# Performance work log

Measured on AMD Instinct MI355X. Metric: run time of the kernel, lower is better.

Reference implementation:

```python
import jax, jax.numpy as jnp
import numpy as np

B, S, D = 64, 4096, 256
LN_EPS = 1e-3  # Keras LayerNormalization default epsilon


def setup_inputs() -> dict:
    key = jax.random.key(0)
    k1, k2, k3 = jax.random.split(key, 3)
    x = jax.random.normal(k1, (B, S, D), dtype=jnp.float32)
    mask = jnp.ones((B, S), dtype=jnp.float32)
    gamma = jnp.ones((D,), dtype=jnp.float32)       # LayerNorm scale
    beta = jnp.zeros((D,), dtype=jnp.float32)       # LayerNorm offset
    w = jax.random.normal(k2, (D,), dtype=jnp.float32) * (1.0 / np.sqrt(D))  # Dense(1) kernel
    b = jnp.zeros((), dtype=jnp.float32)            # Dense(1) bias
    return {"x": x, "mask": mask, "gamma": gamma, "beta": beta, "w": w, "b": b}


def reference(x, mask, gamma, beta, w, b):
    # LayerNorm over feature dim
    mu = jnp.mean(x, axis=-1, keepdims=True)
    var = jnp.mean(jnp.square(x - mu), axis=-1, keepdims=True)
    xn = (x - mu) * jax.lax.rsqrt(var + LN_EPS) * gamma + beta  # [B,S,D]
    # Dense(1) score projection
    score = jnp.einsum('bsd,d->bs', xn, w) + b                  # [B,S]
    # Mask out padded positions, softmax over sequence axis
    score = score + (1.0 - mask) * -1e9
    weights = jax.nn.softmax(score, axis=1)                     # [B,S]
    # Weighted sum over sequence
    return jnp.einsum('bsd,bs->bd', x, weights)                 # [B,D]
```

## Files before the change

kernel.cpp:

```cpp
#include <hip/hip_runtime.h>
#include <math.h>

#define B_   64
#define S_   4096
#define D_   256
#define CH   32
#define ROWS_PER_CHUNK (S_ / CH)
#define NWAVE 4
#define ROWS_PER_BLOCK_ITER (NWAVE * 4)
#define NITER (ROWS_PER_CHUNK / ROWS_PER_BLOCK_ITER)
#define LN_EPS 1e-3f

__global__ __launch_bounds__(256) void pool_pass1(
    const float* __restrict__ x, const float* __restrict__ mask,
    const float* __restrict__ gamma, const float* __restrict__ w,
    float* __restrict__ ws_acc, float* __restrict__ ws_m, float* __restrict__ ws_l)
{
    const int blk   = blockIdx.x;
    const int b     = blk / CH;
    const int chunk = blk % CH;
    const int tid   = threadIdx.x;
    const int lane  = tid & 63;
    const int wave  = tid >> 6;
    const int q     = lane >> 4;
    const int t     = lane & 15;

    float4 gw[4];
    float sgw = 0.0f;
    #pragma unroll
    for (int k = 0; k < 4; ++k) {
        const int d = t * 4 + 64 * k;
        const float4 g4 = *(const float4*)(gamma + d);
        const float4 w4 = *(const float4*)(w + d);
        gw[k].x = g4.x * w4.x; gw[k].y = g4.y * w4.y;
        gw[k].z = g4.z * w4.z; gw[k].w = g4.w * w4.w;
        sgw += gw[k].x + gw[k].y + gw[k].z + gw[k].w;
    }
    #pragma unroll
    for (int off = 8; off > 0; off >>= 1) sgw += __shfl_xor(sgw, off, 64);

    const int row0 = chunk * ROWS_PER_CHUNK + wave * 4 + q;
    const float* xbase = x + ((size_t)b * S_ + row0) * D_ + t * 4;
    const float* mbase = mask + (size_t)b * S_ + row0;

    float  m = -3.0e38f;
    float  l = 0.0f;
    float4 acc[4];
    #pragma unroll
    for (int k = 0; k < 4; ++k) acc[k] = make_float4(0.f, 0.f, 0.f, 0.f);

    float4 v[4];
    #pragma unroll
    for (int k = 0; k < 4; ++k) v[k] = *(const float4*)(xbase + 64 * k);
    float msk = mbase[0];

    for (int i = 0; i < NITER; ++i) {
        const int inx = (i + 1 < NITER) ? i + 1 : i;
        float4 vn[4];
        #pragma unroll
        for (int k = 0; k < 4; ++k)
            vn[k] = *(const float4*)(xbase + (size_t)inx * ROWS_PER_BLOCK_ITER * D_ + 64 * k);
        const float mskn = mbase[inx * ROWS_PER_BLOCK_ITER];

        float s1 = 0.f, s2 = 0.f, s3 = 0.f;
        #pragma unroll
        for (int k = 0; k < 4; ++k) {
            s1 += v[k].x + v[k].y + v[k].z + v[k].w;
            s2 += v[k].x*v[k].x + v[k].y*v[k].y + v[k].z*v[k].z + v[k].w*v[k].w;
            s3 += v[k].x*gw[k].x + v[k].y*gw[k].y + v[k].z*gw[k].z + v[k].w*gw[k].w;
        }
        #pragma unroll
        for (int off = 8; off > 0; off >>= 1) {
            s1 += __shfl_xor(s1, off, 64);
            s2 += __shfl_xor(s2, off, 64);
            s3 += __shfl_xor(s3, off, 64);
        }
        const float mu    = s1 * (1.0f / D_);
        const float var   = s2 * (1.0f / D_) - mu * mu;
        const float rstd  = rsqrtf(var + LN_EPS);
        const float score = rstd * (s3 - mu * sgw) + (1.0f - msk) * -1e9f;

        const float mnew  = fmaxf(m, score);
        const float scale = __expf(m - mnew);
        const float p     = __expf(score - mnew);
        m = mnew;
        l = l * scale + p;
        #pragma unroll
        for (int k = 0; k < 4; ++k) {
            acc[k].x = acc[k].x * scale + p * v[k].x;
            acc[k].y = acc[k].y * scale + p * v[k].y;
            acc[k].z = acc[k].z * scale + p * v[k].z;
            acc[k].w = acc[k].w * scale + p * v[k].w;
        }

        #pragma unroll
        for (int k = 0; k < 4; ++k) v[k] = vn[k];
        msk = mskn;
    }

    __shared__ float s_acc[NWAVE * 4][D_];
    __shared__ float s_m[NWAVE * 4];
    __shared__ float s_l[NWAVE * 4];
    const int g = wave * 4 + q;
    #pragma unroll
    for (int k = 0; k < 4; ++k) *(float4*)&s_acc[g][t * 4 + 64 * k] = acc[k];
    if (t == 0) { s_m[g] = m; s_l[g] = l; }
    __syncthreads();

    float M = -3.0e38f;
    #pragma unroll
    for (int gg = 0; gg < 16; ++gg) M = fmaxf(M, s_m[gg]);
    float L = 0.f, a = 0.f;
    #pragma unroll
    for (int gg = 0; gg < 16; ++gg) {
        const float e = __expf(s_m[gg] - M);
        L += e * s_l[gg];
        a += e * s_acc[gg][tid];
    }
    ws_acc[(size_t)blk * D_ + tid] = a;
    if (tid == 0) { ws_m[blk] = M; ws_l[blk] = L; }
}

__global__ __launch_bounds__(256) void pool_pass2(
    const float* __restrict__ ws_acc, const float* __restrict__ ws_m,
    const float* __restrict__ ws_l, float* __restrict__ out)
{
    const int b = blockIdx.x;
    const int d = threadIdx.x;

    float M = -3.0e38f;
    #pragma unroll
    for (int c = 0; c < CH; ++c) M = fmaxf(M, ws_m[b * CH + c]);

    float L = 0.0f, a = 0.0f;
    #pragma unroll
    for (int c = 0; c < CH; ++c) {
        const float e = __expf(ws_m[b * CH + c] - M);
        L += e * ws_l[b * CH + c];
        a += e * ws_acc[((size_t)(b * CH + c)) * D_ + d];
    }
    out[(size_t)b * D_ + d] = a / L;
}

extern "C" void kernel_launch(void* const* d_in, const int* in_sizes, int n_in,
                              void* d_out, int out_size, void* d_ws, size_t ws_size,
                              hipStream_t stream) {
    const float* x     = (const float*)d_in[0];
    const float* mask  = (const float*)d_in[1];
    const float* gamma = (const float*)d_in[2];
    const float* w     = (const float*)d_in[4];
    float* out = (float*)d_out;

    float* ws_acc = (float*)d_ws;
    float* ws_m   = ws_acc + (size_t)B_ * CH * D_;
    float* ws_l   = ws_m + B_ * CH;

    pool_pass1<<<B_ * CH, 256, 0, stream>>>(x, mask, gamma, w, ws_acc, ws_m, ws_l);
    pool_pass2<<<B_, 256, 0, stream>>>(ws_acc, ws_m, ws_l, out);
}
```

Before: 363.0 us.

## Fuse split-softmax combine into pass1 via last-block atomic counter

Merges the two-kernel split reduction into one kernel. Each block bumps a per-batch atomic counter after writing its partial result, and the last block to finish for that batch does the final cross-chunk combine, which removes the second kernel launch. It also switches the x loads to nontemporal loads and uses ext_vector_type math. A memset of the counters is added on the stream each call, plus threadfence overhead.

```diff
diff --git a/kernel.cpp b/kernel.cpp
--- a/kernel.cpp
+++ b/kernel.cpp
@@ -11,10 +11,13 @@
 #define NITER (ROWS_PER_CHUNK / ROWS_PER_BLOCK_ITER)
 #define LN_EPS 1e-3f
 
-__global__ __launch_bounds__(256) void pool_pass1(
+typedef float f4 __attribute__((ext_vector_type(4)));
+
+__global__ __launch_bounds__(256) void pool_fused(
     const float* __restrict__ x, const float* __restrict__ mask,
     const float* __restrict__ gamma, const float* __restrict__ w,
-    float* __restrict__ ws_acc, float* __restrict__ ws_m, float* __restrict__ ws_l)
+    float* __restrict__ ws_acc, float* __restrict__ ws_m, float* __restrict__ ws_l,
+    int* __restrict__ ws_cnt, float* __restrict__ out)
 {
     const int blk   = blockIdx.x;
     const int b     = blk / CH;
@@ -25,16 +28,15 @@
     const int q     = lane >> 4;
     const int t     = lane & 15;
 
-    float4 gw[4];
+    f4 gw[4];
     float sgw = 0.0f;
     #pragma unroll
     for (int k = 0; k < 4; ++k) {
         const int d = t * 4 + 64 * k;
-        const float4 g4 = *(const float4*)(gamma + d);
-        const float4 w4 = *(const float4*)(w + d);
-        gw[k].x = g4.x * w4.x; gw[k].y = g4.y * w4.y;
-        gw[k].z = g4.z * w4.z; gw[k].w = g4.w * w4.w;
-        sgw += gw[k].x + gw[k].y + gw[k].z + gw[k].w;
+        const f4 g4 = *(const f4*)(gamma + d);
+        const f4 w4 = *(const f4*)(w + d);
+        gw[k] = g4 * w4;
+        sgw += gw[k][0] + gw[k][1] + gw[k][2] + gw[k][3];
     }
     #pragma unroll
     for (int off = 8; off > 0; off >>= 1) sgw += __shfl_xor(sgw, off, 64);
@@ -43,31 +45,33 @@
     const float* xbase = x + ((size_t)b * S_ + row0) * D_ + t * 4;
     const float* mbase = mask + (size_t)b * S_ + row0;
 
-    float  m = -3.0e38f;
-    float  l = 0.0f;
-    float4 acc[4];
+    float m = -3.0e38f;
+    float l = 0.0f;
+    f4 acc[4];
     #pragma unroll
-    for (int k = 0; k < 4; ++k) acc[k] = make_float4(0.f, 0.f, 0.f, 0.f);
+    for (int k = 0; k < 4; ++k) acc[k] = (f4)0.0f;
 
-    float4 v[4];
+    f4 v[4];
     #pragma unroll
-    for (int k = 0; k < 4; ++k) v[k] = *(const float4*)(xbase + 64 * k);
+    for (int k = 0; k < 4; ++k)
+        v[k] = __builtin_nontemporal_load((const f4*)(xbase + 64 * k));
     float msk = mbase[0];
 
     for (int i = 0; i < NITER; ++i) {
         const int inx = (i + 1 < NITER) ? i + 1 : i;
-        float4 vn[4];
+        f4 vn[4];
         #pragma unroll
         for (int k = 0; k < 4; ++k)
-            vn[k] = *(const float4*)(xbase + (size_t)inx * ROWS_PER_BLOCK_ITER * D_ + 64 * k);
+            vn[k] = __builtin_nontemporal_load(
+                (const f4*)(xbase + (size_t)inx * ROWS_PER_BLOCK_ITER * D_ + 64 * k));
         const float mskn = mbase[inx * ROWS_PER_BLOCK_ITER];
 
         float s1 = 0.f, s2 = 0.f, s3 = 0.f;
         #pragma unroll
         for (int k = 0; k < 4; ++k) {
-            s1 += v[k].x + v[k].y + v[k].z + v[k].w;
-            s2 += v[k].x*v[k].x + v[k].y*v[k].y + v[k].z*v[k].z + v[k].w*v[k].w;
-            s3 += v[k].x*gw[k].x + v[k].y*gw[k].y + v[k].z*gw[k].z + v[k].w*gw[k].w;
+            s1 += v[k][0] + v[k][1] + v[k][2] + v[k][3];
+            s2 += v[k][0]*v[k][0] + v[k][1]*v[k][1] + v[k][2]*v[k][2] + v[k][3]*v[k][3];
+            s3 += v[k][0]*gw[k][0] + v[k][1]*gw[k][1] + v[k][2]*gw[k][2] + v[k][3]*gw[k][3];
         }
         #pragma unroll
         for (int off = 8; off > 0; off >>= 1) {
@@ -86,12 +90,7 @@
         m = mnew;
         l = l * scale + p;
         #pragma unroll
-        for (int k = 0; k < 4; ++k) {
-            acc[k].x = acc[k].x * scale + p * v[k].x;
-            acc[k].y = acc[k].y * scale + p * v[k].y;
-            acc[k].z = acc[k].z * scale + p * v[k].z;
-            acc[k].w = acc[k].w * scale + p * v[k].w;
-        }
+        for (int k = 0; k < 4; ++k) acc[k] = acc[k] * scale + p * v[k];
 
         #pragma unroll
         for (int k = 0; k < 4; ++k) v[k] = vn[k];
@@ -103,7 +102,7 @@
     __shared__ float s_l[NWAVE * 4];
     const int g = wave * 4 + q;
     #pragma unroll
-    for (int k = 0; k < 4; ++k) *(float4*)&s_acc[g][t * 4 + 64 * k] = acc[k];
+    for (int k = 0; k < 4; ++k) *(f4*)&s_acc[g][t * 4 + 64 * k] = acc[k];
     if (t == 0) { s_m[g] = m; s_l[g] = l; }
     __syncthreads();
 
@@ -119,27 +118,26 @@
     }
     ws_acc[(size_t)blk * D_ + tid] = a;
     if (tid == 0) { ws_m[blk] = M; ws_l[blk] = L; }
-}
 
-__global__ __launch_bounds__(256) void pool_pass2(
-    const float* __restrict__ ws_acc, const float* __restrict__ ws_m,
-    const float* __restrict__ ws_l, float* __restrict__ out)
-{
-    const int b = blockIdx.x;
-    const int d = threadIdx.x;
+    __threadfence();
+    __shared__ int s_is_last;
+    if (tid == 0)
+        s_is_last = (atomicAdd(&ws_cnt[b], 1) == CH - 1);
+    __syncthreads();
+    if (!s_is_last) return;
+    __threadfence();
 
-    float M = -3.0e38f;
+    float M2 = -3.0e38f;
     #pragma unroll
-    for (int c = 0; c < CH; ++c) M = fmaxf(M, ws_m[b * CH + c]);
-
-    float L = 0.0f, a = 0.0f;
+    for (int c = 0; c < CH; ++c) M2 = fmaxf(M2, ws_m[b * CH + c]);
+    float L2 = 0.f, a2 = 0.f;
     #pragma unroll
     for (int c = 0; c < CH; ++c) {
-        const float e = __expf(ws_m[b * CH + c] - M);
-        L += e * ws_l[b * CH + c];
-        a += e * ws_acc[((size_t)(b * CH + c)) * D_ + d];
+        const float e = __expf(ws_m[b * CH + c] - M2);
+        L2 += e * ws_l[b * CH + c];
+        a2 += e * ws_acc[((size_t)(b * CH + c)) * D_ + tid];
     }
-    out[(size_t)b * D_ + d] = a / L;
+    out[(size_t)b * D_ + tid] = a2 / L2;
 }
 
 extern "C" void kernel_launch(void* const* d_in, const int* in_sizes, int n_in,
@@ -154,7 +152,10 @@
     float* ws_acc = (float*)d_ws;
     float* ws_m   = ws_acc + (size_t)B_ * CH * D_;
     float* ws_l   = ws_m + B_ * CH;
+    int*   ws_cnt = (int*)(ws_l + B_ * CH);
 
-    pool_pass1<<<B_ * CH, 256, 0, stream>>>(x, mask, gamma, w, ws_acc, ws_m, ws_l);
-    pool_pass2<<<B_, 256, 0, stream>>>(ws_acc, ws_m, ws_l, out);
+    hipMemsetAsync(ws_cnt, 0, B_ * sizeof(int), stream);
+
+    pool_fused<<<B_ * CH, 256, 0, stream>>>(x, mask, gamma, w,
+                                            ws_acc, ws_m, ws_l, ws_cnt, out);
 }
```

New measurement: 799.4 us. 120% more time.
